# Kernel tuning notes

Measured on AMD Instinct MI355X. Metric: run time of the kernel, lower is better.

Reference implementation:

```python
import jax, jax.numpy as jnp
import numpy as np

DECAY = 0.99
EPS = 1e-6


def setup_inputs() -> dict:
    key = jax.random.key(0)
    k1, k2, k3, k4 = jax.random.split(key, 4)
    B, L, D, K = 32, 1024, 512, 8192
    return {
        "z_e": jax.random.normal(k1, (B, L, D), dtype=jnp.float32),
        "codebook": jax.random.normal(k2, (K, D), dtype=jnp.float32),
        "cluster_size": jax.random.uniform(k3, (K,), dtype=jnp.float32),
        "ema_w": jax.random.normal(k4, (K, D), dtype=jnp.float32),
    }


def reference(z_e, codebook, cluster_size, ema_w):
    B, L, D = z_e.shape
    K = codebook.shape[0]
    flat = z_e.reshape(-1, D)  # [N, D], N = B*L

    dist = ((flat * flat).sum(1, keepdims=True)
            - 2.0 * flat @ codebook.T
            + (codebook * codebook).sum(1))
    idx = jnp.argmin(dist, axis=1)  # [N]
    z_q = codebook[idx].reshape(B, L, D)

    # EMA statistics (training-mode buffer update); one-hot scatter -> segment_sum
    counts = jax.ops.segment_sum(jnp.ones((B * L,), flat.dtype), idx, num_segments=K)
    dw = jax.ops.segment_sum(flat, idx, num_segments=K)  # [K, D]
    new_cluster_size = DECAY * cluster_size + (1.0 - DECAY) * counts
    new_ema_w = DECAY * ema_w + (1.0 - DECAY) * dw
    n = new_cluster_size.sum()
    cs = (new_cluster_size + EPS) / (n + K * EPS) * n  # Laplace-smoothed counts
    new_codebook = new_ema_w / cs[:, None]

    # loss = mse(sg(z_q), z_e) + 0.25 * mse(z_e, sg(z_q)) = 1.25 * mse
    zq_sg = jax.lax.stop_gradient(z_q)
    loss = 1.25 * jnp.mean((z_e - zq_sg) ** 2)

    # straight-through estimator
    z_q_st = z_e + jax.lax.stop_gradient(z_q - z_e)
    return z_q_st, idx.reshape(B, L), loss, new_codebook, new_cluster_size, new_ema_w
```

## Files before the change

kernel.cpp:

```cpp
#include <hip/hip_runtime.h>


constexpr int N = 32768;
constexpr int D = 512;
constexpr int K = 8192;
constexpr int CAP  = 8192;
constexpr int CAPE = 4096;

constexpr float DECAYF  = 0.99f;
constexpr float OMDECAY = (float)(1.0 - 0.99);
constexpr float EPSF    = 1e-6f;
constexpr float KEPSF   = (float)(8192 * 1e-6);
constexpr float TAU1    = 1.0f;
constexpr float TAU2    = 0.02f;

typedef unsigned int       u32;
typedef unsigned short     u16;
typedef unsigned long long u64;
typedef float  f32x4 __attribute__((ext_vector_type(4)));
typedef u32    u32x4 __attribute__((ext_vector_type(4)));
typedef __bf16 bf16x8 __attribute__((ext_vector_type(8)));

#define AS1 __attribute__((address_space(1)))
#define AS3 __attribute__((address_space(3)))

constexpr size_t OFF_CNORM  = 0;
constexpr size_t OFF_IDX    = OFF_CNORM + K;
constexpr size_t OFF_CNTI   = OFF_IDX + N;
constexpr size_t OFF_FLAGC  = OFF_CNTI + K;
constexpr size_t OFF_FLAG2C = OFF_FLAGC + 1;
constexpr size_t OFF_NEXT   = OFF_FLAG2C + 1;
constexpr size_t OFF_OFFS   = OFF_NEXT + K;
constexpr size_t OFF_LIST   = OFF_OFFS + K + 1;
constexpr size_t OFF_FLAGL  = OFF_LIST + N;
constexpr size_t OFF_FLAG2L = OFF_FLAGL + CAP;
constexpr size_t OFF_PB1    = OFF_FLAG2L + N;
constexpr size_t OFF_PB2    = OFF_PB1 + 16 * CAP;
constexpr size_t OFF_PI1    = OFF_PB2 + 16 * CAP;
constexpr size_t OFF_ESLOT  = (OFF_PI1 + 16 * CAP + 1) & ~(size_t)1;
constexpr size_t OFF_SUMS   = (OFF_ESLOT + 2 * CAPE + 1) & ~(size_t)1;
constexpr size_t OFF_LOSSP  = (OFF_SUMS + 2 + 1) & ~(size_t)1;
constexpr size_t OFF_CBH    = (OFF_LOSSP + 2 * K + 3) & ~(size_t)3;
static_assert((OFF_ESLOT & 1) == 0 && (OFF_SUMS & 1) == 0 && (OFF_LOSSP & 1) == 0, "align");
static_assert((OFF_CBH & 3) == 0, "16B align for global_load_lds");

constexpr size_t OUT_ZQ   = 0;
constexpr size_t OUT_IDX  = OUT_ZQ + (size_t)N * D;
constexpr size_t OUT_LOSS = OUT_IDX + N;
constexpr size_t OUT_NCB  = OUT_LOSS + 1;
constexpr size_t OUT_NCS  = OUT_NCB + (size_t)K * D;
constexpr size_t OUT_EMA  = OUT_NCS + K;
constexpr size_t XH_F  = OUT_ZQ;
constexpr size_t PX2_F = OUT_ZQ + (size_t)N * 256;

__device__ inline u16 f32_to_bf16_rne(float f)
{
    u32 u = __builtin_bit_cast(u32, f);
    u = (u + 0x7FFFu + ((u >> 16) & 1u)) >> 16;
    return (u16)u;
}

__global__ __launch_bounds__(256) void split_hi_kernel(const float* __restrict__ src,
                                                       u32x4* __restrict__ dst)
{
    const int T = blockIdx.x;
    const int w = threadIdx.x >> 6;
    const int l = threadIdx.x & 63;
    const int row = T * 16 + (l & 15);
#pragma unroll
    for (int i = 0; i < 4; ++i) {
        const int S  = w * 4 + i;
        const int q4 = S * 8 + (l >> 4) * 2;
        const float4 va = ((const float4*)src)[(size_t)row * 128 + q4];
        const float4 vb = ((const float4*)src)[(size_t)row * 128 + q4 + 1];
        const float a[8] = {va.x, va.y, va.z, va.w, vb.x, vb.y, vb.z, vb.w};
        u32x4 o;
#pragma unroll
        for (int j = 0; j < 4; ++j)
            ((u32*)&o)[j] = (u32)f32_to_bf16_rne(a[2 * j]) |
                            ((u32)f32_to_bf16_rne(a[2 * j + 1]) << 16);
        dst[((size_t)T * 16 + S) * 64 + l] = o;
    }
}

__global__ __launch_bounds__(256) void split_int_kernel(const float* __restrict__ src,
                                                        u32x4* __restrict__ dst)
{
    const int R = blockIdx.x;
    const int w = threadIdx.x >> 6;
    const int l = threadIdx.x & 63;
    const int row = R * 16 + (l & 15);
    const int cq  = l >> 4;
#pragma unroll
    for (int i = 0; i < 8; ++i) {
        const int S = w + 4 * i;
        const float4 v = ((const float4*)src)[(size_t)row * 128 + S * 4 + cq];
        u32x4 o;
        const float a[4] = {v.x, v.y, v.z, v.w};
#pragma unroll
        for (int j = 0; j < 4; ++j) {
            const u16 hi = f32_to_bf16_rne(a[j]);
            const float hif = __builtin_bit_cast(float, (u32)hi << 16);
            const u16 lo = f32_to_bf16_rne(a[j] - hif);
            ((u32*)&o)[j] = (u32)hi | ((u32)lo << 16);
        }
        dst[((size_t)R * 32 + S) * 64 + l] = o;
    }
}

__global__ __launch_bounds__(256) void repack_kernel(
    const float* __restrict__ z_e, const int* __restrict__ flag_cnt,
    const int* __restrict__ flag_list, u32x4* __restrict__ PX2)
{
    const int B = blockIdx.x;
    const int cnt = min(*flag_cnt, CAP);
    if (B * 16 >= cnt) return;
    const int w = threadIdx.x >> 6;
    const int l = threadIdx.x & 63;
    const int srow = B * 16 + (l & 15);
    const int n = (srow < cnt) ? (flag_list[srow] & (N - 1)) : 0;
    const int cq = l >> 4;
#pragma unroll
    for (int i = 0; i < 8; ++i) {
        const int S = w + 4 * i;
        const float4 v = ((const float4*)z_e)[(size_t)n * 128 + S * 4 + cq];
        u32x4 o;
        const float a[4] = {v.x, v.y, v.z, v.w};
#pragma unroll
        for (int j = 0; j < 4; ++j) {
            const u16 hi = f32_to_bf16_rne(a[j]);
            const float hif = __builtin_bit_cast(float, (u32)hi << 16);
            const u16 lo = f32_to_bf16_rne(a[j] - hif);
            ((u32*)&o)[j] = (u32)hi | ((u32)lo << 16);
        }
        PX2[((size_t)B * 32 + S) * 64 + l] = o;
    }
}

__global__ __launch_bounds__(256) void row_norm_kernel(const float* __restrict__ a,
                                                       float* __restrict__ out)
{
    const int row  = blockIdx.x * 4 + (threadIdx.x >> 6);
    const int lane = threadIdx.x & 63;
    const float4* r = (const float4*)(a + (size_t)row * D);
    const float4 v0 = r[lane];
    const float4 v1 = r[lane + 64];
    float s = v0.x * v0.x + v0.y * v0.y + v0.z * v0.z + v0.w * v0.w
            + v1.x * v1.x + v1.y * v1.y + v1.z * v1.z + v1.w * v1.w;
#pragma unroll
    for (int m = 32; m >= 1; m >>= 1) s += __shfl_xor(s, m, 64);
    if (lane == 0) out[row] = s;
}

constexpr int BPH = 128, BCH = 512, KIH = 64;
constexpr int NSTEPH = 512 / KIH;
constexpr int NCHUNKH = K / BCH;
constexpr int TOTH = NCHUNKH * NSTEPH;
constexpr int CELH = BCH * KIH;
constexpr int XELH = BPH * KIH;
constexpr int BUFH = CELH + XELH;

__global__ __launch_bounds__(512, 2) void argmin_hi_kernel(
    const u16* __restrict__ CBH, const u16* __restrict__ XH,
    const float* __restrict__ cnorm,
    int* __restrict__ idx_i, float* __restrict__ idx_f,
    int* __restrict__ flag_cnt, int* __restrict__ flag_list,
    int* __restrict__ flag2_cnt, int* __restrict__ flag2_list)
{
    __shared__ __align__(16) u16 lds[2][BUFH];

    const int tid  = threadIdx.x;
    const int w    = tid >> 6;
    const int lane = tid & 63;
    const int lhi  = lane >> 4;
    const int n0   = blockIdx.x * BPH;

    u32 cbo[8], xo[2];
#pragma unroll
    for (int m = 0; m < 8; ++m) {
        const int flat = m * 512 + tid;
        cbo[m] = (u32)((flat >> 7) * 8192 + (flat & 127) * 8);
    }
#pragma unroll
    for (int m = 0; m < 2; ++m) {
        const int flat = m * 512 + tid;
        xo[m] = (u32)((n0 / 16 + (flat >> 7)) * 8192 + (flat & 127) * 8);
    }

    auto stage = [&](int parity) {
        u16* bufp = &lds[parity][0];
#pragma unroll
        for (int m = 0; m < 8; ++m) {
            __builtin_amdgcn_global_load_lds((const AS1 u32*)(CBH + cbo[m]),
                (AS3 u32*)(bufp + (m * 512 + tid) * 8), 16, 0, 0);
            cbo[m] += 1024;
        }
#pragma unroll
        for (int m = 0; m < 2; ++m) {
            __builtin_amdgcn_global_load_lds((const AS1 u32*)(XH + xo[m]),
                (AS3 u32*)(bufp + CELH + (m * 512 + tid) * 8), 16, 0, 0);
            xo[m] += 1024;
        }
    };

    float b1[8], b2[8]; int i1[8];
#pragma unroll
    for (int p = 0; p < 8; ++p) { b1[p] = INFINITY; b2[p] = INFINITY; i1[p] = 0; }

    stage(0);
    __syncthreads();
    int sc = 1;

    for (int chunk = 0; chunk < NCHUNKH; ++chunk) {
        f32x4 acc[4][8];
        const f32x4 zero = {0.f, 0.f, 0.f, 0.f};
#pragma unroll
        for (int cg = 0; cg < 4; ++cg)
#pragma unroll
            for (int p = 0; p < 8; ++p) acc[cg][p] = zero;

        for (int s8 = 0; s8 < NSTEPH; ++s8) {
            const u16* cur = &lds[s8 & 1][0];
            if (sc < TOTH) {
                if ((sc & (NSTEPH - 1)) == 0) {
#pragma unroll
                    for (int m = 0; m < 8; ++m) cbo[m] += 262144 - 8192;
#pragma unroll
                    for (int m = 0; m < 2; ++m) xo[m] -= 8192;
                }
                stage(sc & 1);
                ++sc;
            }
#pragma unroll
            for (int sl = 0; sl < 2; ++sl) {
                u32x4 bfr[8];
#pragma unroll
                for (int p = 0; p < 8; ++p)
                    bfr[p] = *(const u32x4*)(cur + CELH + p * 1024 + sl * 512 + lane * 8);
#pragma unroll
                for (int cg = 0; cg < 4; ++cg) {
                    const u32x4 af = *(const u32x4*)(cur + (w * 4 + cg) * 1024
                                                     + sl * 512 + lane * 8);
#pragma unroll
                    for (int p = 0; p < 8; ++p)
                        acc[cg][p] = __builtin_amdgcn_mfma_f32_16x16x32_bf16(
                            __builtin_bit_cast(bf16x8, af),
                            __builtin_bit_cast(bf16x8, bfr[p]), acc[cg][p], 0, 0, 0);
                }
            }
            __syncthreads();
        }

        const int cb0 = chunk * BCH + w * 64;
#pragma unroll
        for (int cg = 0; cg < 4; ++cg) {
            const int code0 = cb0 + cg * 16 + lhi * 4;
            const float4 cn4 = *(const float4*)(cnorm + code0);
            const float cn[4] = {cn4.x, cn4.y, cn4.z, cn4.w};
#pragma unroll
            for (int p = 0; p < 8; ++p) {
                const f32x4 A = acc[cg][p];
                const float dv[4] = {cn[0] - 2.f * A.x, cn[1] - 2.f * A.y,
                                     cn[2] - 2.f * A.z, cn[3] - 2.f * A.w};
#pragma unroll
                for (int r = 0; r < 4; ++r) {
                    if (dv[r] < b1[p]) { b2[p] = b1[p]; b1[p] = dv[r]; i1[p] = code0 + r; }
                    else if (dv[r] < b2[p]) { b2[p] = dv[r]; }
                }
            }
        }
    }

#pragma unroll
    for (int p = 0; p < 8; ++p) {
#pragma unroll
        for (int m = 16; m <= 32; m <<= 1) {
            const float ob1 = __shfl_xor(b1[p], m, 64);
            const float ob2 = __shfl_xor(b2[p], m, 64);
            const int   oi1 = __shfl_xor(i1[p], m, 64);
            const float nb2 = fminf(fminf(b2[p], ob2), fmaxf(b1[p], ob1));
            if (ob1 < b1[p] || (ob1 == b1[p] && oi1 < i1[p])) { b1[p] = ob1; i1[p] = oi1; }
            b2[p] = nb2;
        }
    }

    __syncthreads();

    float* mb1 = (float*)&lds[0][0];
    float* mb2 = mb1 + 8 * BPH;
    int*   mi  = (int*)(mb2 + 8 * BPH);
    if (lane < 16) {
#pragma unroll
        for (int p = 0; p < 8; ++p) {
            const int pt = p * 16 + lane;
            mb1[w * BPH + pt] = b1[p];
            mb2[w * BPH + pt] = b2[p];
            mi [w * BPH + pt] = i1[p];
        }
    }
    __syncthreads();
    if (tid < BPH) {
        float fb1 = INFINITY, fb2 = INFINITY; int fi = 0;
        for (int ww = 0; ww < 8; ++ww) {
            const float a1 = mb1[ww * BPH + tid], a2 = mb2[ww * BPH + tid];
            const int   ai = mi[ww * BPH + tid];
            const float nb2 = fminf(fminf(fb2, a2), fmaxf(fb1, a1));
            if (a1 < fb1 || (a1 == fb1 && ai < fi)) { fb1 = a1; fi = ai; }
            fb2 = nb2;
        }
        const int n = n0 + tid;
        idx_i[n] = fi;
        idx_f[n] = (float)fi;
        if (fb2 - fb1 < TAU1) {
            const int pos = atomicAdd(flag_cnt, 1);
            if (pos < CAP) flag_list[pos] = n;
            else {
                const int p2 = atomicAdd(flag2_cnt, 1);
                if ((unsigned)p2 < (unsigned)N) flag2_list[p2] = n;
            }
        }
    }
}

constexpr int CEL2 = 512 * 32;
constexpr int XEL2 = 128 * 32;
constexpr int BUF2 = CEL2 + XEL2;

__global__ __launch_bounds__(512, 2) void argmin_part_kernel(
    const u16* __restrict__ CB2, const u16* __restrict__ PX2,
    const float* __restrict__ cnorm, const int* __restrict__ flag_cnt,
    float* __restrict__ pb1, float* __restrict__ pb2, int* __restrict__ pi1)
{
    const int q  = blockIdx.x & 15;
    const int sb = blockIdx.x >> 4;
    const int cnt = min(*flag_cnt, CAP);
    if (sb * 128 >= cnt) return;
    const int n0s = sb * 128;

    __shared__ __align__(16) u16 lds[2][BUF2];

    const int tid  = threadIdx.x;
    const int w    = tid >> 6;
    const int lane = tid & 63;
    const int lhi  = lane >> 4;

    auto stage = [&](u16* bufp, int s) {
#pragma unroll
        for (int j = 0; j < 4; ++j) {
            const int slot = j * 512 + tid;
            const u16* gsrc = CB2 + (((size_t)(q * 32 + (slot >> 6)) * 32 + s) * 512
                                     + (slot & 63) * 8);
            __builtin_amdgcn_global_load_lds((const AS1 u32*)gsrc,
                                             (AS3 u32*)(bufp + slot * 8), 16, 0, 0);
        }
        const u16* gx = PX2 + (((size_t)(n0s / 16 + (tid >> 6)) * 32 + s) * 512
                               + (tid & 63) * 8);
        __builtin_amdgcn_global_load_lds((const AS1 u32*)gx,
                                         (AS3 u32*)(bufp + CEL2 + tid * 8), 16, 0, 0);
    };

    float b1[8], b2[8]; int i1[8];
#pragma unroll
    for (int p = 0; p < 8; ++p) { b1[p] = INFINITY; b2[p] = INFINITY; i1[p] = 0; }

    f32x4 acc[4][8];
    const f32x4 zero = {0.f, 0.f, 0.f, 0.f};
#pragma unroll
    for (int cg = 0; cg < 4; ++cg)
#pragma unroll
        for (int p = 0; p < 8; ++p) acc[cg][p] = zero;

    stage(&lds[0][0], 0);
    __syncthreads();

#pragma unroll 2
    for (int s = 0; s < 32; ++s) {
        const u16* cur = (s & 1) ? &lds[1][0] : &lds[0][0];
        u16* nxt       = (s & 1) ? &lds[0][0] : &lds[1][0];
        if (s + 1 < 32) stage(nxt, s + 1);

        u32x4 bfr[8];
#pragma unroll
        for (int p = 0; p < 8; ++p)
            bfr[p] = *(const u32x4*)(cur + CEL2 + p * 512 + lane * 8);
#pragma unroll
        for (int cg = 0; cg < 4; ++cg) {
            const u32x4 af = *(const u32x4*)(cur + (w * 4 + cg) * 512 + lane * 8);
            u32x4 as;
            as.x = (af.x >> 16) | (af.x << 16);
            as.y = (af.y >> 16) | (af.y << 16);
            as.z = (af.z >> 16) | (af.z << 16);
            as.w = (af.w >> 16) | (af.w << 16);
#pragma unroll
            for (int p = 0; p < 8; ++p) {
                acc[cg][p] = __builtin_amdgcn_mfma_f32_16x16x32_bf16(
                    __builtin_bit_cast(bf16x8, af), __builtin_bit_cast(bf16x8, bfr[p]),
                    acc[cg][p], 0, 0, 0);
                acc[cg][p] = __builtin_amdgcn_mfma_f32_16x16x32_bf16(
                    __builtin_bit_cast(bf16x8, as), __builtin_bit_cast(bf16x8, bfr[p]),
                    acc[cg][p], 0, 0, 0);
            }
        }
        __syncthreads();
    }

    const int cb0 = q * 512 + w * 64;
#pragma unroll
    for (int cg = 0; cg < 4; ++cg) {
        const int code0 = cb0 + cg * 16 + lhi * 4;
        const float4 cn4 = *(const float4*)(cnorm + code0);
        const float cn[4] = {cn4.x, cn4.y, cn4.z, cn4.w};
#pragma unroll
        for (int p = 0; p < 8; ++p) {
            const f32x4 A = acc[cg][p];
            const float dv[4] = {cn[0] - 2.f * A.x, cn[1] - 2.f * A.y,
                                 cn[2] - 2.f * A.z, cn[3] - 2.f * A.w};
#pragma unroll
            for (int r = 0; r < 4; ++r) {
                if (dv[r] < b1[p]) { b2[p] = b1[p]; b1[p] = dv[r]; i1[p] = code0 + r; }
                else if (dv[r] < b2[p]) { b2[p] = dv[r]; }
            }
        }
    }

#pragma unroll
    for (int p = 0; p < 8; ++p) {
#pragma unroll
        for (int m = 16; m <= 32; m <<= 1) {
            const float ob1 = __shfl_xor(b1[p], m, 64);
            const float ob2 = __shfl_xor(b2[p], m, 64);
            const int   oi1 = __shfl_xor(i1[p], m, 64);
            const float nb2 = fminf(fminf(b2[p], ob2), fmaxf(b1[p], ob1));
            if (ob1 < b1[p] || (ob1 == b1[p] && oi1 < i1[p])) { b1[p] = ob1; i1[p] = oi1; }
            b2[p] = nb2;
        }
    }

    __syncthreads();

    float* mb1 = (float*)&lds[0][0];
    float* mb2 = mb1 + 8 * 128;
    int*   mi  = (int*)(mb2 + 8 * 128);
    if (lane < 16) {
#pragma unroll
        for (int p = 0; p < 8; ++p) {
            const int pt = p * 16 + lane;
            mb1[w * 128 + pt] = b1[p];
            mb2[w * 128 + pt] = b2[p];
            mi [w * 128 + pt] = i1[p];
        }
    }
    __syncthreads();
    if (tid < 128) {
        float fb1 = INFINITY, fb2 = INFINITY; int fi = 0;
        for (int ww = 0; ww < 8; ++ww) {
            const float a1 = mb1[ww * 128 + tid], a2 = mb2[ww * 128 + tid];
            const int   ai = mi[ww * 128 + tid];
            const float nb2 = fminf(fminf(fb2, a2), fmaxf(fb1, a1));
            if (a1 < fb1 || (a1 == fb1 && ai < fi)) { fb1 = a1; fi = ai; }
            fb2 = nb2;
        }
        const int slot = n0s + tid;
        pb1[q * CAP + slot] = fb1;
        pb2[q * CAP + slot] = fb2;
        pi1[q * CAP + slot] = fi;
    }
}

__global__ __launch_bounds__(256) void combine_kernel(
    const int* __restrict__ flag_cnt, const int* __restrict__ flag_list,
    const float* __restrict__ pb1, const float* __restrict__ pb2,
    const int* __restrict__ pi1,
    int* __restrict__ idx_i, float* __restrict__ idx_f,
    int* __restrict__ flag2_cnt, int* __restrict__ flag2_list)
{
    const int s = blockIdx.x * 256 + threadIdx.x;
    const int cnt = min(*flag_cnt, CAP);
    if (s >= cnt) return;
    float fb1 = INFINITY, fb2 = INFINITY; int fi = 0x7fffffff;
#pragma unroll
    for (int q = 0; q < 16; ++q) {
        const float a1 = pb1[q * CAP + s], a2 = pb2[q * CAP + s];
        const int   ai = pi1[q * CAP + s];
        const float nb2 = fminf(fminf(fb2, a2), fmaxf(fb1, a1));
        if (a1 < fb1 || (a1 == fb1 && ai < fi)) { fb1 = a1; fi = ai; }
        fb2 = nb2;
    }
    const int n = flag_list[s] & (N - 1);
    idx_i[n] = fi;
    idx_f[n] = (float)fi;
    if (fb2 - fb1 < TAU2) {
        const int p2 = atomicAdd(flag2_cnt, 1);
        if ((unsigned)p2 < (unsigned)N) flag2_list[p2] = n;
    }
}

__global__ __launch_bounds__(256) void exact_part_kernel(
    const float* __restrict__ x, const float* __restrict__ cb,
    const float* __restrict__ cnorm, const int* __restrict__ flag2_cnt,
    const int* __restrict__ flag2_list, u64* __restrict__ eslot)
{
    __shared__ float4 xs[128];
    __shared__ u64 red[256];
    const int cnt = min(*flag2_cnt, CAPE);
    const int nwork = cnt * 16;
    for (int j = blockIdx.x; j < nwork; j += gridDim.x) {
        const int s = j >> 4;
        const int q = j & 15;
        const int n = flag2_list[s] & (N - 1);
        __syncthreads();
        if (threadIdx.x < 128)
            xs[threadIdx.x] = ((const float4*)(x + (size_t)n * D))[threadIdx.x];
        __syncthreads();
        u64 bestp = ~0ull;
#pragma unroll
        for (int c = 0; c < 2; ++c) {
            const int k = q * 512 + c * 256 + threadIdx.x;
            const float4* crow = (const float4*)(cb + (size_t)k * D);
            float a0 = 0.f, a1 = 0.f, a2 = 0.f, a3 = 0.f;
            for (int d = 0; d < 128; ++d) {
                const float4 xv = xs[d], cv = crow[d];
                a0 = fmaf(xv.x, cv.x, a0);
                a1 = fmaf(xv.y, cv.y, a1);
                a2 = fmaf(xv.z, cv.z, a2);
                a3 = fmaf(xv.w, cv.w, a3);
            }
            const float dist = cnorm[k] - 2.0f * ((a0 + a1) + (a2 + a3));
            u32 ub = __builtin_bit_cast(u32, dist);
            ub = (ub & 0x80000000u) ? ~ub : (ub | 0x80000000u);
            const u64 pk = ((u64)ub << 32) | (u32)k;
            bestp = bestp < pk ? bestp : pk;
        }
        red[threadIdx.x] = bestp;
        __syncthreads();
        for (int off = 128; off > 0; off >>= 1) {
            if (threadIdx.x < off) {
                const u64 o = red[threadIdx.x + off];
                if (o < red[threadIdx.x]) red[threadIdx.x] = o;
            }
            __syncthreads();
        }
        if (threadIdx.x == 0) atomicMin(&eslot[s], red[0]);
    }
}

__global__ __launch_bounds__(256) void exact_write_kernel(
    const int* __restrict__ flag2_cnt, const int* __restrict__ flag2_list,
    const u64* __restrict__ eslot, int* __restrict__ idx_i, float* __restrict__ idx_f)
{
    const int s = blockIdx.x * 256 + threadIdx.x;
    const int cnt = min(*flag2_cnt, CAPE);
    if (s >= cnt) return;
    const int n = flag2_list[s] & (N - 1);
    const int k = (int)(eslot[s] & (u64)(K - 1));
    idx_i[n] = k;
    idx_f[n] = (float)k;
}

__global__ __launch_bounds__(256) void count_kernel(
    const int* __restrict__ idx_i, int* __restrict__ cnti)
{
    const int p = blockIdx.x * 256 + threadIdx.x;
    atomicAdd(&cnti[idx_i[p] & (K - 1)], 1);
}

__global__ __launch_bounds__(256) void scan_kernel(
    const int* __restrict__ cnti, const float* __restrict__ csz,
    int* __restrict__ offs, int* __restrict__ nxt,
    float* __restrict__ ncs, double* __restrict__ n_sum)
{
    __shared__ int    tsum[256];
    __shared__ double dsum[256];
    const int t = threadIdx.x;
    const int base = t * 32;
    int s = 0;
    double dn = 0.0;
#pragma unroll
    for (int i = 0; i < 32; ++i) {
        const int c = cnti[base + i];
        s += c;
        const float v = DECAYF * csz[base + i] + OMDECAY * (float)c;
        ncs[base + i] = v;
        dn += (double)v;
    }
    tsum[t] = s; dsum[t] = dn;
    __syncthreads();
    int run = 0;
    for (int j = 0; j < t; ++j) run += tsum[j];
#pragma unroll
    for (int i = 0; i < 32; ++i) {
        offs[base + i] = run;
        nxt[base + i] = run;
        run += cnti[base + i];
    }
    if (t == 255) offs[K] = run;
    if (t == 0) {
        double tot = 0.0;
        for (int j = 0; j < 256; ++j) tot += dsum[j];
        n_sum[0] = tot;
    }
}

__global__ __launch_bounds__(256) void fill_kernel(
    const int* __restrict__ idx_i, int* __restrict__ nxt, int* __restrict__ list)
{
    const int p = blockIdx.x * 256 + threadIdx.x;
    const int k = idx_i[p] & (K - 1);
    const int pos = atomicAdd(&nxt[k], 1);
    if ((unsigned)pos < (unsigned)N) list[pos] = p;
}

__global__ __launch_bounds__(128) void gather_finalize_kernel(
    const float* __restrict__ x, const float* __restrict__ cb,
    const int* __restrict__ offs, const int* __restrict__ list,
    const float* __restrict__ ema_w, const float* __restrict__ ncs,
    const double* __restrict__ n_sum, float* __restrict__ new_ema,
    float* __restrict__ new_cb, float* __restrict__ zq,
    double* __restrict__ loss_part)
{
    const int k = blockIdx.x;
    const int t = threadIdx.x;
    const int beg = min(offs[k], N), end = min(offs[k + 1], N);
    const size_t o = (size_t)k * 128 + t;
    const float4 c = ((const float4*)cb)[o];
    float4 acc = {0.f, 0.f, 0.f, 0.f};
    float lsum = 0.f;
    for (int i = beg; i < end; ++i) {
        const int p = list[i] & (N - 1);
        const float4 v = ((const float4*)x)[(size_t)p * 128 + t];
        acc.x += v.x; acc.y += v.y; acc.z += v.z; acc.w += v.w;
        ((float4*)zq)[(size_t)p * 128 + t] = c;
        const float d0 = v.x - c.x, d1 = v.y - c.y, d2 = v.z - c.z, d3 = v.w - c.w;
        lsum += d0 * d0 + d1 * d1 + d2 * d2 + d3 * d3;
    }
    const float n = (float)n_sum[0];
    const float csm = (ncs[k] + EPSF) / (n + KEPSF) * n;
    const float4 e = ((const float4*)ema_w)[o];
    float4 ne;
    ne.x = DECAYF * e.x + OMDECAY * acc.x;
    ne.y = DECAYF * e.y + OMDECAY * acc.y;
    ne.z = DECAYF * e.z + OMDECAY * acc.z;
    ne.w = DECAYF * e.w + OMDECAY * acc.w;
    ((float4*)new_ema)[o] = ne;
    float4 nc;
    nc.x = ne.x / csm; nc.y = ne.y / csm; nc.z = ne.z / csm; nc.w = ne.w / csm;
    ((float4*)new_cb)[o] = nc;

#pragma unroll
    for (int m = 32; m >= 1; m >>= 1) lsum += __shfl_xor(lsum, m, 64);
    __shared__ float prt[2];
    if ((t & 63) == 0) prt[t >> 6] = lsum;
    __syncthreads();
    if (t == 0) loss_part[k] = (double)(prt[0] + prt[1]);
}

__global__ __launch_bounds__(256) void loss_reduce_kernel(
    const double* __restrict__ loss_part, float* __restrict__ out_loss)
{
    __shared__ double red[256];
    const int t = threadIdx.x;
    double s = 0.0;
    for (int i = t; i < K; i += 256) s += loss_part[i];
    red[t] = s;
    __syncthreads();
    for (int off = 128; off > 0; off >>= 1) {
        if (t < off) red[t] += red[t + off];
        __syncthreads();
    }
    if (t == 0)
        out_loss[0] = (float)(1.25 * (red[0] / (double)((size_t)N * D)));
}

extern "C" void kernel_launch(void* const* d_in, const int* in_sizes, int n_in,
                              void* d_out, int out_size, void* d_ws, size_t ws_size,
                              hipStream_t stream)
{
    const float* z_e   = (const float*)d_in[0];
    const float* cbook = (const float*)d_in[1];
    const float* csz   = (const float*)d_in[2];
    const float* ema_w = (const float*)d_in[3];

    float* out = (float*)d_out;
    u32*   ws  = (u32*)d_ws;

    float*  cnorm      = (float*)(ws + OFF_CNORM);
    int*    idx_i      = (int*)(ws + OFF_IDX);
    int*    cnti       = (int*)(ws + OFF_CNTI);
    int*    flag_cnt   = (int*)(ws + OFF_FLAGC);
    int*    flag2_cnt  = (int*)(ws + OFF_FLAG2C);
    int*    nxt        = (int*)(ws + OFF_NEXT);
    int*    offs       = (int*)(ws + OFF_OFFS);
    int*    list       = (int*)(ws + OFF_LIST);
    int*    flag_list  = (int*)(ws + OFF_FLAGL);
    int*    flag2_list = (int*)(ws + OFF_FLAG2L);
    float*  pb1        = (float*)(ws + OFF_PB1);
    float*  pb2        = (float*)(ws + OFF_PB2);
    int*    pi1        = (int*)(ws + OFF_PI1);
    u64*    eslot      = (u64*)(ws + OFF_ESLOT);
    double* n_sum      = (double*)(ws + OFF_SUMS);
    double* loss_part  = (double*)(ws + OFF_LOSSP);
    u16*    CBH        = (u16*)(ws + OFF_CBH);

    u16* XH  = (u16*)(out + XH_F);
    u16* PX2 = (u16*)(out + PX2_F);
    u16* CB2 = (u16*)(out + OUT_NCB);

    hipMemsetAsync(ws + OFF_CNTI, 0, (K + 2) * sizeof(u32), stream);
    hipMemsetAsync(ws + OFF_ESLOT, 0xFF, CAPE * sizeof(u64), stream);

    split_hi_kernel<<<N / 16, 256, 0, stream>>>(z_e, (u32x4*)XH);
    split_hi_kernel<<<K / 16, 256, 0, stream>>>(cbook, (u32x4*)CBH);
    split_int_kernel<<<K / 16, 256, 0, stream>>>(cbook, (u32x4*)CB2);
    row_norm_kernel<<<K / 4, 256, 0, stream>>>(cbook, cnorm);

    argmin_hi_kernel<<<N / BPH, 512, 0, stream>>>(CBH, XH, cnorm, idx_i,
                                                  out + OUT_IDX, flag_cnt, flag_list,
                                                  flag2_cnt, flag2_list);

    repack_kernel<<<CAP / 16, 256, 0, stream>>>(z_e, flag_cnt, flag_list, (u32x4*)PX2);

    argmin_part_kernel<<<(CAP / 128) * 16, 512, 0, stream>>>(CB2, PX2, cnorm, flag_cnt,
                                                             pb1, pb2, pi1);

    combine_kernel<<<CAP / 256, 256, 0, stream>>>(flag_cnt, flag_list, pb1, pb2, pi1,
                                                  idx_i, out + OUT_IDX,
                                                  flag2_cnt, flag2_list);

    exact_part_kernel<<<2048, 256, 0, stream>>>(z_e, cbook, cnorm, flag2_cnt,
                                                flag2_list, eslot);

    exact_write_kernel<<<CAPE / 256, 256, 0, stream>>>(flag2_cnt, flag2_list, eslot,
                                                       idx_i, out + OUT_IDX);

    count_kernel<<<N / 256, 256, 0, stream>>>(idx_i, cnti);

    scan_kernel<<<1, 256, 0, stream>>>(cnti, csz, offs, nxt, out + OUT_NCS, n_sum);

    fill_kernel<<<N / 256, 256, 0, stream>>>(idx_i, nxt, list);

    gather_finalize_kernel<<<K, 128, 0, stream>>>(z_e, cbook, offs, list, ema_w,
                                                  out + OUT_NCS, n_sum,
                                                  out + OUT_EMA, out + OUT_NCB,
                                                  out + OUT_ZQ, loss_part);

    loss_reduce_kernel<<<1, 256, 0, stream>>>(loss_part, out + OUT_LOSS);
}
```

Before: 841.3 us.

## Split bf16 argmin over four codebook quarters and merge partial top-2 results

```diff
diff --git a/kernel.cpp b/kernel.cpp
--- a/kernel.cpp
+++ b/kernel.cpp
@@ -52,6 +52,9 @@
 constexpr size_t OUT_EMA  = OUT_NCS + K;
 constexpr size_t XH_F  = OUT_ZQ;
 constexpr size_t PX2_F = OUT_ZQ + (size_t)N * 256;
+constexpr size_t PB1H_F = OUT_EMA;
+constexpr size_t PB2H_F = OUT_EMA + 4 * (size_t)N;
+constexpr size_t PI1H_F = OUT_EMA + 8 * (size_t)N;
 
 __device__ inline u16 f32_to_bf16_rne(float f)
 {
@@ -154,8 +157,8 @@
 
 constexpr int BPH = 128, BCH = 512, KIH = 64;
 constexpr int NSTEPH = 512 / KIH;
-constexpr int NCHUNKH = K / BCH;
-constexpr int TOTH = NCHUNKH * NSTEPH;
+constexpr int NCHQ   = 4;
+constexpr int TOTQ   = NCHQ * NSTEPH;
 constexpr int CELH = BCH * KIH;
 constexpr int XELH = BPH * KIH;
 constexpr int BUFH = CELH + XELH;
@@ -163,23 +166,23 @@
 __global__ __launch_bounds__(512, 2) void argmin_hi_kernel(
     const u16* __restrict__ CBH, const u16* __restrict__ XH,
     const float* __restrict__ cnorm,
-    int* __restrict__ idx_i, float* __restrict__ idx_f,
-    int* __restrict__ flag_cnt, int* __restrict__ flag_list,
-    int* __restrict__ flag2_cnt, int* __restrict__ flag2_list)
+    float* __restrict__ pb1h, float* __restrict__ pb2h, int* __restrict__ pi1h)
 {
     __shared__ __align__(16) u16 lds[2][BUFH];
 
+    const int b    = blockIdx.x;
+    const int kq   = (b & 7) >> 1;
+    const int n0   = ((b >> 3) * 2 + (b & 1)) * BPH;
     const int tid  = threadIdx.x;
     const int w    = tid >> 6;
     const int lane = tid & 63;
     const int lhi  = lane >> 4;
-    const int n0   = blockIdx.x * BPH;
 
     u32 cbo[8], xo[2];
 #pragma unroll
     for (int m = 0; m < 8; ++m) {
         const int flat = m * 512 + tid;
-        cbo[m] = (u32)((flat >> 7) * 8192 + (flat & 127) * 8);
+        cbo[m] = (u32)(kq * 1048576 + (flat >> 7) * 8192 + (flat & 127) * 8);
     }
 #pragma unroll
     for (int m = 0; m < 2; ++m) {
@@ -211,7 +214,7 @@
     __syncthreads();
     int sc = 1;
 
-    for (int chunk = 0; chunk < NCHUNKH; ++chunk) {
+    for (int cc = 0; cc < NCHQ; ++cc) {
         f32x4 acc[4][8];
         const f32x4 zero = {0.f, 0.f, 0.f, 0.f};
 #pragma unroll
@@ -221,7 +224,7 @@
 
         for (int s8 = 0; s8 < NSTEPH; ++s8) {
             const u16* cur = &lds[s8 & 1][0];
-            if (sc < TOTH) {
+            if (sc < TOTQ) {
                 if ((sc & (NSTEPH - 1)) == 0) {
 #pragma unroll
                     for (int m = 0; m < 8; ++m) cbo[m] += 262144 - 8192;
@@ -251,7 +254,8 @@
             __syncthreads();
         }
 
-        const int cb0 = chunk * BCH + w * 64;
+        const int gchunk = kq * NCHQ + cc;
+        const int cb0 = gchunk * BCH + w * 64;
 #pragma unroll
         for (int cg = 0; cg < 4; ++cg) {
             const int code0 = cb0 + cg * 16 + lhi * 4;
@@ -309,15 +313,37 @@
             fb2 = nb2;
         }
         const int n = n0 + tid;
-        idx_i[n] = fi;
-        idx_f[n] = (float)fi;
-        if (fb2 - fb1 < TAU1) {
-            const int pos = atomicAdd(flag_cnt, 1);
-            if (pos < CAP) flag_list[pos] = n;
-            else {
-                const int p2 = atomicAdd(flag2_cnt, 1);
-                if ((unsigned)p2 < (unsigned)N) flag2_list[p2] = n;
-            }
+        pb1h[kq * N + n] = fb1;
+        pb2h[kq * N + n] = fb2;
+        pi1h[kq * N + n] = fi;
+    }
+}
+
+__global__ __launch_bounds__(256) void merge_hi_kernel(
+    const float* __restrict__ pb1h, const float* __restrict__ pb2h,
+    const int* __restrict__ pi1h,
+    int* __restrict__ idx_i, float* __restrict__ idx_f,
+    int* __restrict__ flag_cnt, int* __restrict__ flag_list,
+    int* __restrict__ flag2_cnt, int* __restrict__ flag2_list)
+{
+    const int n = blockIdx.x * 256 + threadIdx.x;
+    float fb1 = INFINITY, fb2 = INFINITY; int fi = 0x7fffffff;
+#pragma unroll
+    for (int q = 0; q < 4; ++q) {
+        const float a1 = pb1h[q * N + n], a2 = pb2h[q * N + n];
+        const int   ai = pi1h[q * N + n];
+        const float nb2 = fminf(fminf(fb2, a2), fmaxf(fb1, a1));
+        if (a1 < fb1 || (a1 == fb1 && ai < fi)) { fb1 = a1; fi = ai; }
+        fb2 = nb2;
+    }
+    idx_i[n] = fi;
+    idx_f[n] = (float)fi;
+    if (fb2 - fb1 < TAU1) {
+        const int pos = atomicAdd(flag_cnt, 1);
+        if (pos < CAP) flag_list[pos] = n;
+        else {
+            const int p2 = atomicAdd(flag2_cnt, 1);
+            if ((unsigned)p2 < (unsigned)N) flag2_list[p2] = n;
         }
     }
 }
@@ -704,6 +730,9 @@
     u16* XH  = (u16*)(out + XH_F);
     u16* PX2 = (u16*)(out + PX2_F);
     u16* CB2 = (u16*)(out + OUT_NCB);
+    float* pb1h = out + PB1H_F;
+    float* pb2h = out + PB2H_F;
+    int*   pi1h = (int*)(out + PI1H_F);
 
     hipMemsetAsync(ws + OFF_CNTI, 0, (K + 2) * sizeof(u32), stream);
     hipMemsetAsync(ws + OFF_ESLOT, 0xFF, CAPE * sizeof(u64), stream);
@@ -713,9 +742,12 @@
     split_int_kernel<<<K / 16, 256, 0, stream>>>(cbook, (u32x4*)CB2);
     row_norm_kernel<<<K / 4, 256, 0, stream>>>(cbook, cnorm);
 
-    argmin_hi_kernel<<<N / BPH, 512, 0, stream>>>(CBH, XH, cnorm, idx_i,
-                                                  out + OUT_IDX, flag_cnt, flag_list,
-                                                  flag2_cnt, flag2_list);
+    argmin_hi_kernel<<<(N / BPH) * 4, 512, 0, stream>>>(CBH, XH, cnorm,
+                                                        pb1h, pb2h, pi1h);
+
+    merge_hi_kernel<<<N / 256, 256, 0, stream>>>(pb1h, pb2h, pi1h, idx_i,
+                                                 out + OUT_IDX, flag_cnt, flag_list,
+                                                 flag2_cnt, flag2_list);
 
     repack_kernel<<<CAP / 16, 256, 0, stream>>>(z_e, flag_cnt, flag_list, (u32x4*)PX2);
 
```

After: 861.8 us. 2.4% more time.
